# Kernel tuning notes

Measured on AMD Instinct MI355X. Metric: run time of the kernel, lower is better.

The kernel has to match this reference:

```python
import jax, jax.numpy as jnp
import numpy as np

N_HEAD = 6
NEG_INF = -1e9


def _structural_masks(adj, distance):
    """Build the 6 per-head structural masks (B, 6, L, L) bool.

    Heads: [self-loop only, 1-hop (adj), 2-hop reachable, distance<=2,
            distance<=3, global]. Inferred from the 6-signal docstring;
    preprocess_adj adds self loops and binarizes.
    """
    B, L, _ = adj.shape
    eye = jnp.eye(L, dtype=bool)[None]                      # (1, L, L)
    a1 = (adj > 0) | eye                                    # 1-hop + self
    a1f = a1.astype(jnp.float32)
    a2 = (jnp.einsum('blm,bmn->bln', a1f, a1f) > 0)         # 2-hop reachable
    d2 = distance <= 2
    d3 = distance <= 3
    full = jnp.ones((B, L, L), dtype=bool)
    return jnp.stack([jnp.broadcast_to(eye, (B, L, L)), a1, a2, d2, d3, full], axis=1)


def setup_inputs() -> dict:
    key = jax.random.key(0)
    k1, k2, k3, k4, k5 = jax.random.split(key, 5)
    B, L, C = 8, 1024, 768
    x = jax.random.normal(k1, (B, L, C), dtype=jnp.float32)
    adj = jax.random.randint(k2, (B, L, L), 0, 2, dtype=jnp.int32)
    distance = jax.random.randint(k3, (B, L, L), 0, 9, dtype=jnp.int32)
    w_qkv = jax.random.normal(k4, (3 * C, C), dtype=jnp.float32) * 0.02
    w_proj = jax.random.normal(k5, (C, C), dtype=jnp.float32) * 0.02
    return {"x": x, "adj": adj, "distance": distance, "w_qkv": w_qkv, "w_proj": w_proj}


def reference(x, adj, distance, w_qkv, w_proj):
    B, L, C = x.shape
    H = N_HEAD
    d = C // H
    scale = jnp.sqrt(jnp.float32(d))

    qkv = x @ w_qkv.T                                       # (B, L, 3C)
    q, k, v = jnp.split(qkv, 3, axis=-1)
    q = q.reshape(B, L, H, d).transpose(0, 2, 1, 3)         # (B, H, L, d)
    k = k.reshape(B, L, H, d).transpose(0, 2, 1, 3)
    v = v.reshape(B, L, H, d).transpose(0, 2, 1, 3)

    score = jnp.einsum('bhld,bhmd->bhlm', q, k) / scale     # (B, H, L, L)
    pe = _structural_masks(adj, distance)                   # (B, H, L, L) bool
    score = jnp.where(pe, score, NEG_INF)                   # masked_fill of bias
    attn = jax.nn.softmax(score, axis=-1)
    out = jnp.einsum('bhlm,bhmd->bhld', attn, v)            # (B, H, L, d)
    out = out.transpose(0, 2, 1, 3).reshape(B, L, C)
    return out @ w_proj.T
```

## Files before the change

### kernel.cpp

```cpp
#include <hip/hip_runtime.h>

typedef unsigned short ushort_t;
typedef unsigned int uint_t;
typedef unsigned long long u64;
typedef __attribute__((ext_vector_type(8))) short bf16x8;
typedef __attribute__((ext_vector_type(4))) float f32x4;
typedef __attribute__((ext_vector_type(16))) float f32x16;
typedef __attribute__((ext_vector_type(4))) uint_t u32x4;

#define B_ 8
#define L_ 1024
#define C_ 768
#define H_ 6
#define D_ 128
#define BH_ 48
#define NEGINF (-1e9f)
#define THR_ 8.0f

#define AS1 __attribute__((address_space(1)))
#define AS3 __attribute__((address_space(3)))

__device__ __forceinline__ ushort_t f2bf(float f) {
  uint_t u = __builtin_bit_cast(uint_t, f);
  u += 0x7fffu + ((u >> 16) & 1u);
  return (ushort_t)(u >> 16);
}
__device__ __forceinline__ float bf2f(ushort_t s) {
  uint_t u = ((uint_t)s) << 16;
  return __builtin_bit_cast(float, u);
}

__global__ void cvt_f32_bf16(const float* __restrict__ in, ushort_t* __restrict__ out, int n8) {
  int i = blockIdx.x * 256 + threadIdx.x;
  if (i >= n8) return;
  const float4* p = (const float4*)in + (size_t)i * 2;
  float4 a = p[0], b = p[1];
  uint4 r;
  r.x = (uint_t)f2bf(a.x) | ((uint_t)f2bf(a.y) << 16);
  r.y = (uint_t)f2bf(a.z) | ((uint_t)f2bf(a.w) << 16);
  r.z = (uint_t)f2bf(b.x) | ((uint_t)f2bf(b.y) << 16);
  r.w = (uint_t)f2bf(b.z) | ((uint_t)f2bf(b.w) << 16);
  ((uint4*)out)[i] = r;
}

__global__ __launch_bounds__(256)
void pack_masks(const int* __restrict__ adj, const int* __restrict__ dist,
                u64* __restrict__ a1p, u64* __restrict__ d2p, u64* __restrict__ d3p) {
  int l = blockIdx.x, b = blockIdx.y, t = threadIdx.x;
  size_t base = ((size_t)b * L_ + l) * L_;
  size_t rb = ((size_t)b * L_ + l) * 16;
  #pragma unroll
  for (int it = 0; it < 4; ++it) {
    int c = it * 256 + t;
    int av = adj[base + c];
    int dv = dist[base + c];
    u64 m1 = __ballot((av > 0) || (c == l));
    u64 m2 = __ballot(dv <= 2);
    u64 m3 = __ballot(dv <= 3);
    if ((t & 63) == 0) {
      int w = it * 4 + (t >> 6);
      a1p[rb + w] = m1; d2p[rb + w] = m2; d3p[rb + w] = m3;
    }
  }
}

__global__ __launch_bounds__(64)
void hop2(const u64* __restrict__ a1p, u64* __restrict__ a2p) {
  int tid = blockIdx.x * 64 + threadIdx.x;
  int b = tid >> 10;
  size_t rb = (size_t)tid * 16;
  u64 row[16], acc[16];
  #pragma unroll
  for (int j = 0; j < 16; ++j) { row[j] = a1p[rb + j]; acc[j] = 0ULL; }
  bool done = false;
  #pragma unroll
  for (int mw = 0; mw < 16; ++mw) {
    if (done) continue;
    u64 bits = row[mw];
    while (bits) {
      int tz = __builtin_ctzll(bits); bits &= bits - 1;
      const u64* src = a1p + (((size_t)b << 10) + (mw << 6) + tz) * 16;
      u64 band = ~0ULL;
      #pragma unroll
      for (int j = 0; j < 16; ++j) { acc[j] |= src[j]; band &= acc[j]; }
      if (band == ~0ULL) { done = true; break; }
    }
  }
  #pragma unroll
  for (int j = 0; j < 16; ++j) a2p[rb + j] = acc[j];
}

template<int EPI>
__global__ __launch_bounds__(256)
void gemm_bt(const ushort_t* __restrict__ A, const ushort_t* __restrict__ Bm,
             int N, int K,
             ushort_t* __restrict__ qo, ushort_t* __restrict__ ko,
             ushort_t* __restrict__ vTo, ushort_t* __restrict__ vo,
             float* __restrict__ fo) {
  __shared__ __align__(16) ushort_t As[128 * 64];
  __shared__ __align__(16) ushort_t Bs[128 * 64];
  int t = threadIdx.x;
  int lane = t & 63, lo = lane & 15, hi = lane >> 4;
  int wv = t >> 6, wm = wv >> 1, wn = wv & 1;

  int gx = gridDim.x;
  int nwg = gx * gridDim.y;
  int orig = blockIdx.y * gx + blockIdx.x;
  int cpx = nwg >> 3;
  int wg = (orig & 7) * cpx + (orig >> 3);
  int n0 = (wg % gx) * 128;
  int m0 = (wg / gx) * 128;

  f32x4 acc[4][4];
  #pragma unroll
  for (int mi = 0; mi < 4; ++mi)
    #pragma unroll
    for (int ni = 0; ni < 4; ++ni) acc[mi][ni] = (f32x4){0.f, 0.f, 0.f, 0.f};

  for (int kt = 0; kt < K; kt += 64) {
    #pragma unroll
    for (int i = 0; i < 4; ++i) {
      int u = i * 256 + t;
      int row = u >> 3, c16 = u & 7;
      int sc = c16 ^ (row & 7);
      __builtin_amdgcn_global_load_lds(
          (const AS1 void*)(A + ((size_t)(m0 + row) * K + kt + sc * 8)),
          (AS3 void*)&As[(size_t)u * 8], 16, 0, 0);
      __builtin_amdgcn_global_load_lds(
          (const AS1 void*)(Bm + ((size_t)(n0 + row) * K + kt + sc * 8)),
          (AS3 void*)&Bs[(size_t)u * 8], 16, 0, 0);
    }
    __syncthreads();
    #pragma unroll
    for (int kks = 0; kks < 2; ++kks) {
      bf16x8 af[4], bfr[4];
      #pragma unroll
      for (int mi = 0; mi < 4; ++mi) {
        int r = wm * 64 + mi * 16 + lo;
        af[mi] = *(const bf16x8*)&As[r * 64 + (((kks * 4 + hi) ^ (r & 7)) * 8)];
      }
      #pragma unroll
      for (int ni = 0; ni < 4; ++ni) {
        int r = wn * 64 + ni * 16 + lo;
        bfr[ni] = *(const bf16x8*)&Bs[r * 64 + (((kks * 4 + hi) ^ (r & 7)) * 8)];
      }
      #pragma unroll
      for (int mi = 0; mi < 4; ++mi)
        #pragma unroll
        for (int ni = 0; ni < 4; ++ni)
          acc[mi][ni] = __builtin_amdgcn_mfma_f32_16x16x32_bf16(af[mi], bfr[ni], acc[mi][ni], 0, 0, 0);
    }
    __syncthreads();
  }

  #pragma unroll
  for (int mi = 0; mi < 4; ++mi) {
    int rbase = m0 + wm * 64 + mi * 16 + hi * 4;
    #pragma unroll
    for (int ni = 0; ni < 4; ++ni) {
      int c = n0 + wn * 64 + ni * 16 + lo;
      f32x4 v = acc[mi][ni];
      if (EPI == 0) {
        int sec = c / 768;
        int cc = c - sec * 768;
        int h = cc >> 7, dd = cc & 127;
        #pragma unroll
        for (int j = 0; j < 4; ++j) {
          int r = rbase + j;
          int b = r >> 10, l = r & 1023;
          size_t bh = (size_t)(b * H_ + h);
          if (sec == 0)      qo[(bh * L_ + l) * D_ + dd] = f2bf(v[j] * 0.08838834764831845f);
          else if (sec == 1) ko[(bh * L_ + l) * D_ + dd] = f2bf(v[j]);
          else {
            ushort_t bv = f2bf(v[j]);
            vTo[(bh * D_ + dd) * L_ + l] = bv;
            vo[(bh * L_ + l) * D_ + dd] = bv;
          }
        }
      } else {
        #pragma unroll
        for (int j = 0; j < 4; ++j)
          fo[(size_t)(rbase + j) * N + c] = v[j];
      }
    }
  }
}

__global__ __launch_bounds__(512)
void attn_kernel(const ushort_t* __restrict__ q, const ushort_t* __restrict__ k,
                 const ushort_t* __restrict__ vT, const ushort_t* __restrict__ v,
                 ushort_t* __restrict__ obf,
                 ushort_t* __restrict__ np0, ushort_t* __restrict__ np1,
                 float* __restrict__ ml,
                 const u64* __restrict__ a1p, const u64* __restrict__ a2p,
                 const u64* __restrict__ d2p, const u64* __restrict__ d3p) {
  __shared__ __align__(16) ushort_t Ks[2][32 * 128];
  __shared__ __align__(16) ushort_t Vs[2][128 * 32];
  int t = threadIdx.x;
  int lane = t & 63, lo32 = lane & 31, hi2 = (lane >> 5) & 1, wv = t >> 6;
  int bh = blockIdx.x, qt = blockIdx.y, half = blockIdx.z;
  int b = bh / H_, h = bh - b * H_;
  int qbase = qt * 256;
  int qw = qbase + wv * 32;
  int kvb = half * 512;

  if (h == 0) {
    if (half) return;
    const ushort_t* vp0 = v + ((size_t)bh * L_ + qbase) * D_;
    ushort_t* op0 = obf + ((size_t)b * L_ + qbase) * C_;
    #pragma unroll
    for (int it = 0; it < 8; ++it) {
      int u = it * 512 + t;
      int r = u >> 4, c = (u & 15) * 8;
      *(bf16x8*)(op0 + (size_t)r * C_ + c) = *(const bf16x8*)(vp0 + (size_t)r * D_ + c);
    }
    return;
  }

  const ushort_t* qp = q + (size_t)bh * L_ * D_;
  const ushort_t* kp = k + (size_t)bh * L_ * D_ + (size_t)kvb * D_;
  const ushort_t* vp = vT + (size_t)bh * D_ * L_ + kvb;

  bf16x8 qf[8];
  #pragma unroll
  for (int dt = 0; dt < 8; ++dt)
    qf[dt] = *(const bf16x8*)(qp + (size_t)(qw + lo32) * D_ + dt * 16 + hi2 * 8);

  const u64* mp = (h == 1) ? a1p : (h == 2) ? a2p : (h == 3) ? d2p : d3p;
  bool full = (h == 5);
  const u64* mrow = mp + ((size_t)b * L_ + qw + lo32) * 16 + half * 8;

  float m_run = NEGINF, l_run = 0.f;
  f32x16 acc[4];
  #pragma unroll
  for (int dt = 0; dt < 4; ++dt)
    #pragma unroll
    for (int r = 0; r < 16; ++r) acc[dt][r] = 0.f;

  auto stage = [&](int buf, int ch) {
    int kc0 = ch * 32;
    {
      int row = t >> 4, c16 = t & 15;
      int sc = c16 ^ (row & 15);
      __builtin_amdgcn_global_load_lds(
          (const AS1 void*)(kp + (size_t)(kc0 + row) * D_ + sc * 8),
          (AS3 void*)&Ks[buf][(size_t)t * 8], 16, 0, 0);
    }
    {
      int row = t >> 2, c16 = t & 3;
      int sc = c16 ^ (row & 3);
      __builtin_amdgcn_global_load_lds(
          (const AS1 void*)(vp + (size_t)row * L_ + kc0 + sc * 8),
          (AS3 void*)&Vs[buf][(size_t)t * 8], 16, 0, 0);
    }
  };

  stage(0, 0);
  u64 mw_cur = full ? 0ULL : mrow[0];
  u64 mw_nxt = 0ULL;
  __syncthreads();

  for (int ch = 0; ch < 16; ++ch) {
    int cur = ch & 1;
    if (ch < 15) stage(cur ^ 1, ch + 1);
    if (!full && (ch & 1) == 0 && (ch >> 1) + 1 < 8)
      mw_nxt = mrow[(ch >> 1) + 1];

    const ushort_t* ks = &Ks[cur][0];
    const ushort_t* vs = &Vs[cur][0];
    uint_t mbits = full ? 0xffffffffu : (uint_t)(mw_cur >> ((ch & 1) * 32));

    f32x16 sacc;
    #pragma unroll
    for (int r = 0; r < 16; ++r) sacc[r] = 0.f;
    __builtin_amdgcn_s_setprio(1);
    #pragma unroll
    for (int dt = 0; dt < 8; ++dt) {
      int c16 = (dt * 2 + hi2) ^ (lo32 & 15);
      bf16x8 kf = *(const bf16x8*)&ks[lo32 * 128 + c16 * 8];
      sacc = __builtin_amdgcn_mfma_f32_32x32x16_bf16(kf, qf[dt], sacc, 0, 0, 0);
    }
    __builtin_amdgcn_s_setprio(0);

    float sv[16];
    #pragma unroll
    for (int r = 0; r < 16; ++r) {
      int shift = (r & 3) + 8 * (r >> 2) + hi2 * 4;
      sv[r] = ((mbits >> shift) & 1u) ? sacc[r] : NEGINF;
    }

    float a8[8];
    #pragma unroll
    for (int j = 0; j < 8; ++j) a8[j] = fmaxf(sv[2 * j], sv[2 * j + 1]);
    #pragma unroll
    for (int j = 0; j < 4; ++j) a8[j] = fmaxf(a8[j], a8[j + 4]);
    float pmax = fmaxf(fmaxf(a8[0], a8[1]), fmaxf(a8[2], a8[3]));
    pmax = fmaxf(pmax, __shfl_xor(pmax, 32));

    if (__any(pmax > m_run + THR_)) {
      float mn = fmaxf(m_run, pmax);
      float corr = __expf(m_run - mn);
      l_run *= corr;
      m_run = mn;
      float cT[16];
      #pragma unroll
      for (int r = 0; r < 16; ++r)
        cT[r] = __shfl(corr, (r & 3) + 8 * (r >> 2) + hi2 * 4);
      #pragma unroll
      for (int dt = 0; dt < 4; ++dt)
        #pragma unroll
        for (int r = 0; r < 16; ++r) acc[dt][r] *= cT[r];
    }

    float p[16];
    #pragma unroll
    for (int r = 0; r < 16; ++r) p[r] = __expf(sv[r] - m_run);
    float s8[8];
    #pragma unroll
    for (int j = 0; j < 8; ++j) s8[j] = p[2 * j] + p[2 * j + 1];
    #pragma unroll
    for (int j = 0; j < 4; ++j) s8[j] = s8[j] + s8[j + 4];
    float rs = (s8[0] + s8[1]) + (s8[2] + s8[3]);
    rs += __shfl_xor(rs, 32);
    l_run += rs;

    uint_t ow[8];
    #pragma unroll
    for (int j = 0; j < 8; ++j)
      ow[j] = (uint_t)f2bf(p[2 * j]) | ((uint_t)f2bf(p[2 * j + 1]) << 16);
    uint_t pw[8];
    #pragma unroll
    for (int j = 0; j < 8; ++j) pw[j] = __shfl_xor(ow[j], 32);
    u32x4 pa0 = (u32x4){hi2 ? pw[2] : ow[0], hi2 ? pw[3] : ow[1],
                        hi2 ? ow[2] : pw[0], hi2 ? ow[3] : pw[1]};
    u32x4 pa1 = (u32x4){hi2 ? pw[6] : ow[4], hi2 ? pw[7] : ow[5],
                        hi2 ? ow[6] : pw[4], hi2 ? ow[7] : pw[5]};
    bf16x8 paf0 = __builtin_bit_cast(bf16x8, pa0);
    bf16x8 paf1 = __builtin_bit_cast(bf16x8, pa1);

    __builtin_amdgcn_s_setprio(1);
    #pragma unroll
    for (int dt = 0; dt < 4; ++dt) {
      int vd = dt * 32 + lo32;
      int c16a = hi2 ^ (vd & 3);
      int c16b = (2 + hi2) ^ (vd & 3);
      bf16x8 vfa = *(const bf16x8*)&vs[vd * 32 + c16a * 8];
      bf16x8 vfb = *(const bf16x8*)&vs[vd * 32 + c16b * 8];
      acc[dt] = __builtin_amdgcn_mfma_f32_32x32x16_bf16(paf0, vfa, acc[dt], 0, 0, 0);
      acc[dt] = __builtin_amdgcn_mfma_f32_32x32x16_bf16(paf1, vfb, acc[dt], 0, 0, 0);
    }
    __builtin_amdgcn_s_setprio(0);
    if (ch & 1) mw_cur = mw_nxt;
    __syncthreads();
  }

  if (hi2 == 0) {
    size_t row = (size_t)bh * L_ + qw + lo32;
    float2 v2 = make_float2(m_run, l_run);
    *(float2*)(ml + ((size_t)half * BH_ * L_ + row) * 2) = v2;
  }
  ushort_t* np = half ? np1 : np0;
  #pragma unroll
  for (int dt = 0; dt < 4; ++dt)
    #pragma unroll
    for (int r = 0; r < 16; ++r) {
      int qrow = qw + (r & 3) + 8 * (r >> 2) + hi2 * 4;
      np[((size_t)bh * L_ + qrow) * D_ + dt * 32 + lo32] = f2bf(acc[dt][r]);
    }
}

__global__ __launch_bounds__(256)
void combine(const ushort_t* __restrict__ np0, const ushort_t* __restrict__ np1,
             const float* __restrict__ ml, ushort_t* __restrict__ obf) {
  int bh = blockIdx.x;
  int b = bh / H_, h = bh - b * H_;
  if (h == 0) return;
  int t = threadIdx.x;
  int qi = t >> 4, di = t & 15;
  int qq = blockIdx.y * 16 + qi;
  size_t row = (size_t)bh * L_ + qq;
  float2 ml1 = *(const float2*)(ml + row * 2);
  float2 ml2 = *(const float2*)(ml + ((size_t)BH_ * L_ + row) * 2);
  float M = fmaxf(ml1.x, ml2.x);
  float w1 = __expf(ml1.x - M), w2 = __expf(ml2.x - M);
  float inv = 1.f / (w1 * ml1.y + w2 * ml2.y);
  bf16x8 n1 = *(const bf16x8*)(np0 + row * D_ + di * 8);
  bf16x8 n2 = *(const bf16x8*)(np1 + row * D_ + di * 8);
  ushort_t o[8];
  #pragma unroll
  for (int j = 0; j < 8; ++j)
    o[j] = f2bf((w1 * bf2f((ushort_t)n1[j]) + w2 * bf2f((ushort_t)n2[j])) * inv);
  *(bf16x8*)(obf + ((size_t)b * L_ + qq) * C_ + h * D_ + di * 8) = *(bf16x8*)o;
}

extern "C" void kernel_launch(void* const* d_in, const int* in_sizes, int n_in,
                              void* d_out, int out_size, void* d_ws, size_t ws_size,
                              hipStream_t stream) {
  const float* x     = (const float*)d_in[0];
  const int*   adj   = (const int*)d_in[1];
  const int*   dist  = (const int*)d_in[2];
  const float* wqkv  = (const float*)d_in[3];
  const float* wproj = (const float*)d_in[4];
  float* out = (float*)d_out;
  char* ws = (char*)d_ws;

  const size_t SZ_X   = (size_t)B_ * L_ * C_ * 2;
  const size_t SZ_WQ  = (size_t)3 * C_ * C_ * 2;
  const size_t SZ_WP  = (size_t)C_ * C_ * 2;
  const size_t SZ_QKV = (size_t)BH_ * L_ * D_ * 2;
  const size_t SZ_MSK = (size_t)B_ * L_ * 16 * 8;
  const size_t SZ_ML  = (size_t)2 * BH_ * L_ * 2 * 4;
  size_t off = 0;
  ushort_t* xbf  = (ushort_t*)(ws + off); off += SZ_X;
  ushort_t* wqb  = (ushort_t*)(ws + off); off += SZ_WQ;
  ushort_t* wpb  = (ushort_t*)(ws + off); off += SZ_WP;
  ushort_t* qb   = (ushort_t*)(ws + off); off += SZ_QKV;
  ushort_t* kb   = (ushort_t*)(ws + off); off += SZ_QKV;
  ushort_t* vTb  = (ushort_t*)(ws + off); off += SZ_QKV;
  ushort_t* vb   = (ushort_t*)(ws + off); off += SZ_QKV;
  ushort_t* ob   = (ushort_t*)(ws + off); off += SZ_X;
  u64* a1p = (u64*)(ws + off); off += SZ_MSK;
  u64* a2p = (u64*)(ws + off); off += SZ_MSK;
  u64* d2p = (u64*)(ws + off); off += SZ_MSK;
  u64* d3p = (u64*)(ws + off); off += SZ_MSK;
  ushort_t* np1 = (ushort_t*)(ws + off); off += SZ_QKV;
  float*    mlb = (float*)(ws + off); off += SZ_ML;
  ushort_t* np0 = xbf;
  (void)ws_size; (void)n_in; (void)in_sizes; (void)out_size;

  cvt_f32_bf16<<<(B_ * L_ * C_ / 8 + 255) / 256, 256, 0, stream>>>(x, xbf, B_ * L_ * C_ / 8);
  cvt_f32_bf16<<<(3 * C_ * C_ / 8 + 255) / 256, 256, 0, stream>>>(wqkv, wqb, 3 * C_ * C_ / 8);
  cvt_f32_bf16<<<(C_ * C_ / 8 + 255) / 256, 256, 0, stream>>>(wproj, wpb, C_ * C_ / 8);
  pack_masks<<<dim3(L_, B_), 256, 0, stream>>>(adj, dist, a1p, d2p, d3p);
  hop2<<<B_ * L_ / 64, 64, 0, stream>>>(a1p, a2p);
  gemm_bt<0><<<dim3(3 * C_ / 128, B_ * L_ / 128), 256, 0, stream>>>(
      xbf, wqb, 3 * C_, C_, qb, kb, vTb, vb, nullptr);
  attn_kernel<<<dim3(BH_, L_ / 256, 2), 512, 0, stream>>>(
      qb, kb, vTb, vb, ob, np0, np1, mlb, a1p, a2p, d2p, d3p);
  combine<<<dim3(BH_, L_ / 16), 256, 0, stream>>>(np0, np1, mlb, ob);
  gemm_bt<1><<<dim3(C_ / 128, B_ * L_ / 128), 256, 0, stream>>>(
      ob, wpb, C_, C_, nullptr, nullptr, nullptr, nullptr, out);
}
```

Measured before the change: 203.7 us.

## Transpose V tile through LDS for coalesced vT stores and drop redundant V writes

The QKV GEMM epilogue is split by section. For V heads 1-5, the tile is staged transposed in shared memory, using the freed A/B tiles with an XOR swizzle. It is then written to vT with 16-byte coalesced stores, replacing the old 2-byte stores strided by L. Only head 0 writes the row-major V copy, and heads 1-5 no longer write it, which removes duplicate global writes. This relies on the attention kernel reading row-major V only for head 0 (the self-loop head) and vT only for the other heads, and it adds an extra sync plus LDS traffic.

```diff
diff --git a/kernel.cpp b/kernel.cpp
--- a/kernel.cpp
+++ b/kernel.cpp
@@ -153,36 +153,85 @@
     __syncthreads();
   }
 
-  #pragma unroll
-  for (int mi = 0; mi < 4; ++mi) {
-    int rbase = m0 + wm * 64 + mi * 16 + hi * 4;
-    #pragma unroll
-    for (int ni = 0; ni < 4; ++ni) {
-      int c = n0 + wn * 64 + ni * 16 + lo;
-      f32x4 v = acc[mi][ni];
-      if (EPI == 0) {
-        int sec = c / 768;
-        int cc = c - sec * 768;
-        int h = cc >> 7, dd = cc & 127;
+  if (EPI == 1) {
+    #pragma unroll
+    for (int mi = 0; mi < 4; ++mi) {
+      int rbase = m0 + wm * 64 + mi * 16 + hi * 4;
+      #pragma unroll
+      for (int ni = 0; ni < 4; ++ni) {
+        int c = n0 + wn * 64 + ni * 16 + lo;
+        f32x4 v = acc[mi][ni];
+        #pragma unroll
+        for (int j = 0; j < 4; ++j)
+          fo[(size_t)(rbase + j) * N + c] = v[j];
+      }
+    }
+    return;
+  }
+  int sec = n0 / 768;
+  if (sec < 2) {
+    #pragma unroll
+    for (int mi = 0; mi < 4; ++mi) {
+      int rbase = m0 + wm * 64 + mi * 16 + hi * 4;
+      #pragma unroll
+      for (int ni = 0; ni < 4; ++ni) {
+        int cc = n0 - sec * 768 + wn * 64 + ni * 16 + lo;
+        int hh = cc >> 7, dd = cc & 127;
+        f32x4 v = acc[mi][ni];
         #pragma unroll
         for (int j = 0; j < 4; ++j) {
           int r = rbase + j;
           int b = r >> 10, l = r & 1023;
-          size_t bh = (size_t)(b * H_ + h);
-          if (sec == 0)      qo[(bh * L_ + l) * D_ + dd] = f2bf(v[j] * 0.08838834764831845f);
-          else if (sec == 1) ko[(bh * L_ + l) * D_ + dd] = f2bf(v[j]);
-          else {
-            ushort_t bv = f2bf(v[j]);
-            vTo[(bh * D_ + dd) * L_ + l] = bv;
-            vo[(bh * L_ + l) * D_ + dd] = bv;
-          }
+          size_t bh = (size_t)(b * H_ + hh);
+          if (sec == 0) qo[(bh * L_ + l) * D_ + dd] = f2bf(v[j] * 0.08838834764831845f);
+          else          ko[(bh * L_ + l) * D_ + dd] = f2bf(v[j]);
         }
-      } else {
+      }
+    }
+    return;
+  }
+  int hh = (n0 - 1536) >> 7;
+  int b = m0 >> 10, l0 = m0 & 1023;
+  size_t bh = (size_t)(b * H_ + hh);
+  if (hh == 0) {
+    #pragma unroll
+    for (int mi = 0; mi < 4; ++mi) {
+      int lb = wm * 64 + mi * 16 + hi * 4;
+      #pragma unroll
+      for (int ni = 0; ni < 4; ++ni) {
+        int dd = wn * 64 + ni * 16 + lo;
+        f32x4 v = acc[mi][ni];
         #pragma unroll
         for (int j = 0; j < 4; ++j)
-          fo[(size_t)(rbase + j) * N + c] = v[j];
-      }
-    }
+          vo[(bh * L_ + l0 + lb + j) * D_ + dd] = f2bf(v[j]);
+      }
+    }
+    return;
+  }
+  #pragma unroll
+  for (int mi = 0; mi < 4; ++mi) {
+    int lb = wm * 64 + mi * 16 + hi * 4;
+    #pragma unroll
+    for (int ni = 0; ni < 4; ++ni) {
+      int dd = wn * 64 + ni * 16 + lo;
+      ushort_t* base = (dd < 64) ? As : Bs;
+      f32x4 v = acc[mi][ni];
+      #pragma unroll
+      for (int j = 0; j < 4; ++j) {
+        int byte = (((dd & 63) * 256 + (lb + j) * 2)) ^ ((dd & 7) << 4);
+        *(ushort_t*)((char*)base + byte) = f2bf(v[j]);
+      }
+    }
+  }
+  __syncthreads();
+  #pragma unroll
+  for (int i = 0; i < 8; ++i) {
+    int u = i * 256 + t;
+    int ddl = u >> 4, c16 = u & 15;
+    const ushort_t* base = (ddl < 64) ? As : Bs;
+    int byte = (((ddl & 63) * 256 + c16 * 16)) ^ ((ddl & 7) << 4);
+    bf16x8 val = *(const bf16x8*)((const char*)base + byte);
+    *(bf16x8*)(vTo + (bh * D_ + ddl) * L_ + l0 + c16 * 8) = val;
   }
 }
 
```

After: 183.6 us. -9.9%, faster.
